# Performance work log

Measured on AMD Instinct MI355X. Metric: run time of the kernel, lower is better.

The kernel has to match this reference:

```python
import jax, jax.numpy as jnp
import numpy as np

TOP_K = 2

def setup_inputs() -> dict:
    key = jax.random.key(0)
    k1, k2 = jax.random.split(key)
    x = jax.random.normal(k1, (8, 4096, 4096), dtype=jnp.float32)
    # nn.Linear weight [num_experts, dim]
    gate_w = jax.random.normal(k2, (64, 4096), dtype=jnp.float32) * (1.0 / np.sqrt(4096))
    return {"x": x, "gate_w": gate_w}

def reference(x, gate_w):
    # logits: [B, S, E]
    logits = jnp.einsum('bsd,ed->bse', x, gate_w)
    routing_weights = jax.nn.softmax(logits, axis=-1)
    top_weights, top_indices = jax.lax.top_k(routing_weights, TOP_K)
    top_weights = top_weights / jnp.sum(top_weights, axis=-1, keepdims=True)
    return top_weights, top_indices
```

## Files before the change

kernel.cpp:

```cpp
#include <hip/hip_runtime.h>
#include <hip/hip_bf16.h>
#include <math.h>


typedef __attribute__((ext_vector_type(8))) short short8;
typedef __attribute__((ext_vector_type(4))) float f32x4;

#define TPB 64
#define NCH 64
#define TAU 1e-4f
#define LROW 68

__device__ __forceinline__ void cvt8(const f32x4* v, short8* hi, short8* lo) {
    const float* f = reinterpret_cast<const float*>(v);
#pragma unroll
    for (int j = 0; j < 8; ++j) {
        __hip_bfloat16 h = __float2bfloat16(f[j]);
        float r = f[j] - __bfloat162float(h);
        __hip_bfloat16 l = __float2bfloat16(r);
        (*hi)[j] = (short)*reinterpret_cast<unsigned short*>(&h);
        (*lo)[j] = (short)*reinterpret_cast<unsigned short*>(&l);
    }
}

__global__ void prep_b(const float* __restrict__ gw,
                       short8* __restrict__ bh, short8* __restrict__ bl) {
    const int tid = blockIdx.x * 256 + threadIdx.x;
    const int ln  = tid & 63;
    const int w   = (tid >> 6) & 127;
    const int nt  = tid >> 13;
    const int row = nt * 16 + (ln & 15);
    const int k   = w * 32 + ((ln >> 4) << 3);
    f32x4 v[2];
    v[0] = *reinterpret_cast<const f32x4*>(gw + (long)row * 4096 + k);
    v[1] = *reinterpret_cast<const f32x4*>(gw + (long)row * 4096 + k + 4);
    short8 h, l;
    cvt8(v, &h, &l);
    bh[tid] = h;
    bl[tid] = l;
}

__device__ __forceinline__ void gload16(const void* g, void* l) {
    __builtin_amdgcn_global_load_lds(
        (const __attribute__((address_space(1))) void*)g,
        (__attribute__((address_space(3))) void*)l, 16, 0, 0);
}

#define STAGE(C, BUF) do {                                                    \
    char* aB = AB + (BUF) * 32768;                                            \
    char* bB = aB + 16384;                                                    \
    _Pragma("unroll")                                                         \
    for (int i = 0; i < 4; ++i)                                               \
        gload16(srcA[i] + (long)(C) * 256, aB + (wv * 4 + i) * 1024 + ln * 16); \
    _Pragma("unroll")                                                         \
    for (int i = 0; i < 4; ++i) {                                             \
        const int s  = wv * 4 + i;                                            \
        const int wl = s >> 3, nt = (s >> 1) & 3, hl = s & 1;                 \
        const short8* sp = (hl ? blp : bhp)                                   \
            + ((long)nt * 8192 + (2 * (C) + wl) * 64 + ln);                   \
        gload16(sp, bB + s * 1024 + ln * 16);                                 \
    }                                                                         \
} while (0)

__global__ __launch_bounds__(256, 2)
void router_fused(const float* __restrict__ x,
                  const short8* __restrict__ bhp,
                  const short8* __restrict__ blp,
                  const float* __restrict__ gw,
                  float* __restrict__ out,
                  int M, int K) {
    __shared__ __align__(16) char AB[65536];
    __shared__ int flags[TPB];
    __shared__ double Ld4[4][64];

    const int t  = threadIdx.x;
    const int wv = t >> 6;
    const int ln = t & 63;
    const int fr = ln & 15;
    const int q  = ln >> 4;
    const long tok0 = (long)blockIdx.x * TPB;
    const int phase = blockIdx.x & (NCH - 1);

    const char* srcA[4];
#pragma unroll
    for (int i = 0; i < 4; ++i) {
        const int row  = (wv * 4 + i) * 4 + (ln >> 4);
        const int sl   = ln & 15;
        const int lslot = (sl & 8) | ((sl & 7) ^ (row & 7));
        srcA[i] = (const char*)x + (tok0 + row) * (long)K * 4 + lslot * 16;
    }

    f32x4 acc[4];
#pragma unroll
    for (int nt = 0; nt < 4; ++nt) acc[nt] = (f32x4){0.f, 0.f, 0.f, 0.f};

    STAGE(phase, 0);
    STAGE((phase + 1) & (NCH - 1), 1);

    const int R  = wv * 16 + fr;
    const int rk = R & 7;

    for (int j = 0; j < NCH; ++j) {
        const int c   = (phase + j) & (NCH - 1);
        const int buf = j & 1;
        if (j + 1 < NCH) asm volatile("s_waitcnt vmcnt(8)" ::: "memory");
        else             asm volatile("s_waitcnt vmcnt(0)" ::: "memory");
        __builtin_amdgcn_s_barrier();
        asm volatile("" ::: "memory");
        __builtin_amdgcn_sched_barrier(0);

        {
            const char* aB = AB + buf * 32768 + R * 256;
            const char* bB = AB + buf * 32768 + 16384;
#pragma unroll
            for (int wl = 0; wl < 2; ++wl) {
                f32x4 av[2];
                av[0] = *(const f32x4*)(aB + (wl * 8 + ((q * 2 + 0) ^ rk)) * 16);
                av[1] = *(const f32x4*)(aB + (wl * 8 + ((q * 2 + 1) ^ rk)) * 16);
                short8 ah, al;
                cvt8(av, &ah, &al);
#pragma unroll
                for (int nt = 0; nt < 4; ++nt) {
                    short8 bhv = *(const short8*)(bB + (wl * 8 + nt * 2 + 0) * 1024 + ln * 16);
                    short8 blv = *(const short8*)(bB + (wl * 8 + nt * 2 + 1) * 1024 + ln * 16);
                    acc[nt] = __builtin_amdgcn_mfma_f32_16x16x32_bf16(ah, bhv, acc[nt], 0, 0, 0);
                    acc[nt] = __builtin_amdgcn_mfma_f32_16x16x32_bf16(ah, blv, acc[nt], 0, 0, 0);
                    acc[nt] = __builtin_amdgcn_mfma_f32_16x16x32_bf16(al, bhv, acc[nt], 0, 0, 0);
                    acc[nt] = __builtin_amdgcn_mfma_f32_16x16x32_bf16(al, blv, acc[nt], 0, 0, 0);
                }
            }
        }

        __builtin_amdgcn_sched_barrier(0);
        asm volatile("" ::: "memory");
        __builtin_amdgcn_s_barrier();
        asm volatile("" ::: "memory");
        if (j + 2 < NCH) STAGE((phase + j + 2) & (NCH - 1), buf);
        __builtin_amdgcn_sched_barrier(0);
    }

    __syncthreads();
    float* Ls = (float*)AB;
#pragma unroll
    for (int nt = 0; nt < 4; ++nt)
#pragma unroll
        for (int r = 0; r < 4; ++r)
            Ls[(wv * 16 + q * 4 + r) * LROW + nt * 16 + fr] = acc[nt][r];
    __syncthreads();

    if (t < TPB) {
        const float* row = Ls + (long)t * LROW;
        float m1 = -INFINITY, m2 = -INFINITY, m3 = -INFINITY;
        int i1 = 0, i2 = 0;
#pragma unroll 8
        for (int e = 0; e < 64; ++e) {
            const float v = row[e];
            if (v > m1)      { m3 = m2; m2 = m1; i2 = i1; m1 = v; i1 = e; }
            else if (v > m2) { m3 = m2; m2 = v; i2 = e; }
            else if (v > m3) { m3 = v; }
        }
        const float e2 = expf(m2 - m1);
        const float s  = 1.0f + e2;

        const long g = tok0 + t;
        out[2 * g + 0] = 1.0f / s;
        out[2 * g + 1] = e2 / s;
        float* oi = out + 2 * (long)M;
        oi[2 * g + 0] = (float)i1;
        oi[2 * g + 1] = (float)i2;

        flags[t] = ((m1 - m2) < TAU) | ((m2 - m3) < TAU);
    }
    __syncthreads();

    for (int tk = 0; tk < TPB; ++tk) {
        if (flags[tk]) {
            const float* xr = x + (tok0 + tk) * (long)K + wv * 1024;
            const float* gr = gw + (long)ln * (long)K + wv * 1024;
            double s0 = 0.0, s1 = 0.0, s2 = 0.0, s3 = 0.0;
            for (int k = 0; k < 1024; k += 4) {
                const f32x4 a = *reinterpret_cast<const f32x4*>(xr + k);
                const f32x4 b = *reinterpret_cast<const f32x4*>(gr + k);
                s0 = fma((double)a.x, (double)b.x, s0);
                s1 = fma((double)a.y, (double)b.y, s1);
                s2 = fma((double)a.z, (double)b.z, s2);
                s3 = fma((double)a.w, (double)b.w, s3);
            }
            Ld4[wv][ln] = (s0 + s1) + (s2 + s3);
            __syncthreads();
            if (t == 0) {
                double m1 = -INFINITY, m2 = -INFINITY;
                int i1 = 0, i2 = 0;
                for (int e = 0; e < 64; ++e) {
                    const double v = Ld4[0][e] + Ld4[1][e] + Ld4[2][e] + Ld4[3][e];
                    if (v > m1)      { m2 = m1; i2 = i1; m1 = v; i1 = e; }
                    else if (v > m2) { m2 = v; i2 = e; }
                }
                const double e2 = exp(m2 - m1);
                const double s  = 1.0 + e2;
                const long g = tok0 + tk;
                out[2 * g + 0] = (float)(1.0 / s);
                out[2 * g + 1] = (float)(e2 / s);
                float* oi = out + 2 * (long)M;
                oi[2 * g + 0] = (float)i1;
                oi[2 * g + 1] = (float)i2;
            }
            __syncthreads();
        }
    }
}

extern "C" void kernel_launch(void* const* d_in, const int* in_sizes, int n_in,
                              void* d_out, int out_size, void* d_ws, size_t ws_size,
                              hipStream_t stream) {
    const float* x  = (const float*)d_in[0];
    const float* gw = (const float*)d_in[1];
    float* out = (float*)d_out;

    const int K = 4096;
    const int M = in_sizes[0] / K;
    const int nblocks = M / TPB;

    short8* bh = (short8*)d_ws;
    short8* bl = bh + 32768;

    prep_b<<<128, 256, 0, stream>>>(gw, bh, bl);
    router_fused<<<nblocks, 256, 0, stream>>>(x, bh, bl, gw, out, M, K);
}
```

Before: 206.1 us.

## Switch router GEMM to triple-buffered half-size chunks with one barrier

Halves the K chunk (NCH 128, 32 floats per row per chunk) and replaces the double buffer with a three-slot LDS ring of 16 KB each. The prefetch for chunk j+2 is issued right after the single per-iteration barrier, which removes the second barrier. LDS drops to 48 KB so three blocks can fit per CU, and MFMA sections are raised in wave priority via s_setprio. The cost is more loop iterations with less work each, and the waitcnt depth and buffer indexing have to stay correct.

```diff
diff --git a/kernel.cpp b/kernel.cpp
--- a/kernel.cpp
+++ b/kernel.cpp
@@ -7,7 +7,7 @@
 typedef __attribute__((ext_vector_type(4))) float f32x4;
 
 #define TPB 64
-#define NCH 64
+#define NCH 128
 #define TAU 1e-4f
 #define LROW 68
 
@@ -46,30 +46,29 @@
         (__attribute__((address_space(3))) void*)l, 16, 0, 0);
 }
 
-#define STAGE(C, BUF) do {                                                    \
-    char* aB = AB + (BUF) * 32768;                                            \
-    char* bB = aB + 16384;                                                    \
+#define STAGE(C, MBUF) do {                                                   \
+    char* aB = AB + (MBUF) * 16384;                                           \
+    char* bB = aB + 8192;                                                     \
     _Pragma("unroll")                                                         \
-    for (int i = 0; i < 4; ++i)                                               \
-        gload16(srcA[i] + (long)(C) * 256, aB + (wv * 4 + i) * 1024 + ln * 16); \
+    for (int i = 0; i < 2; ++i)                                               \
+        gload16(srcA[i] + (long)(C) * 128, aB + (wv * 2 + i) * 1024 + ln * 16); \
     _Pragma("unroll")                                                         \
-    for (int i = 0; i < 4; ++i) {                                             \
-        const int s  = wv * 4 + i;                                            \
-        const int wl = s >> 3, nt = (s >> 1) & 3, hl = s & 1;                 \
-        const short8* sp = (hl ? blp : bhp)                                   \
-            + ((long)nt * 8192 + (2 * (C) + wl) * 64 + ln);                   \
+    for (int i = 0; i < 2; ++i) {                                             \
+        const int s  = wv * 2 + i;                                            \
+        const short8* sp = ((s & 1) ? blp : bhp)                              \
+            + ((long)(s >> 1) * 8192 + (long)(C) * 64 + ln);                  \
         gload16(sp, bB + s * 1024 + ln * 16);                                 \
     }                                                                         \
 } while (0)
 
-__global__ __launch_bounds__(256, 2)
+__global__ __launch_bounds__(256, 3)
 void router_fused(const float* __restrict__ x,
                   const short8* __restrict__ bhp,
                   const short8* __restrict__ blp,
                   const float* __restrict__ gw,
                   float* __restrict__ out,
                   int M, int K) {
-    __shared__ __align__(16) char AB[65536];
+    __shared__ __align__(16) char AB[49152];
     __shared__ int flags[TPB];
     __shared__ double Ld4[4][64];
 
@@ -81,13 +80,12 @@
     const long tok0 = (long)blockIdx.x * TPB;
     const int phase = blockIdx.x & (NCH - 1);
 
-    const char* srcA[4];
-#pragma unroll
-    for (int i = 0; i < 4; ++i) {
-        const int row  = (wv * 4 + i) * 4 + (ln >> 4);
-        const int sl   = ln & 15;
-        const int lslot = (sl & 8) | ((sl & 7) ^ (row & 7));
-        srcA[i] = (const char*)x + (tok0 + row) * (long)K * 4 + lslot * 16;
+    const char* srcA[2];
+#pragma unroll
+    for (int i = 0; i < 2; ++i) {
+        const int row  = (wv * 2 + i) * 8 + (ln >> 3);
+        const int slot = (ln & 7) ^ (row & 7);
+        srcA[i] = (const char*)x + (tok0 + row) * (long)K * 4 + slot * 16;
     }
 
     f32x4 acc[4];
@@ -101,42 +99,37 @@
     const int rk = R & 7;
 
     for (int j = 0; j < NCH; ++j) {
-        const int c   = (phase + j) & (NCH - 1);
-        const int buf = j & 1;
-        if (j + 1 < NCH) asm volatile("s_waitcnt vmcnt(8)" ::: "memory");
+        const int c = (phase + j) & (NCH - 1);
+        const int m = j % 3;
+        if (j < NCH - 1) asm volatile("s_waitcnt vmcnt(4)" ::: "memory");
         else             asm volatile("s_waitcnt vmcnt(0)" ::: "memory");
         __builtin_amdgcn_s_barrier();
         asm volatile("" ::: "memory");
+        if (j + 2 < NCH) STAGE((phase + j + 2) & (NCH - 1), (j + 2) % 3);
         __builtin_amdgcn_sched_barrier(0);
 
         {
-            const char* aB = AB + buf * 32768 + R * 256;
-            const char* bB = AB + buf * 32768 + 16384;
-#pragma unroll
-            for (int wl = 0; wl < 2; ++wl) {
-                f32x4 av[2];
-                av[0] = *(const f32x4*)(aB + (wl * 8 + ((q * 2 + 0) ^ rk)) * 16);
-                av[1] = *(const f32x4*)(aB + (wl * 8 + ((q * 2 + 1) ^ rk)) * 16);
-                short8 ah, al;
-                cvt8(av, &ah, &al);
-#pragma unroll
-                for (int nt = 0; nt < 4; ++nt) {
-                    short8 bhv = *(const short8*)(bB + (wl * 8 + nt * 2 + 0) * 1024 + ln * 16);
-                    short8 blv = *(const short8*)(bB + (wl * 8 + nt * 2 + 1) * 1024 + ln * 16);
-                    acc[nt] = __builtin_amdgcn_mfma_f32_16x16x32_bf16(ah, bhv, acc[nt], 0, 0, 0);
-                    acc[nt] = __builtin_amdgcn_mfma_f32_16x16x32_bf16(ah, blv, acc[nt], 0, 0, 0);
-                    acc[nt] = __builtin_amdgcn_mfma_f32_16x16x32_bf16(al, bhv, acc[nt], 0, 0, 0);
-                    acc[nt] = __builtin_amdgcn_mfma_f32_16x16x32_bf16(al, blv, acc[nt], 0, 0, 0);
-                }
+            const char* aB = AB + m * 16384 + R * 128;
+            const char* bB = AB + m * 16384 + 8192;
+            f32x4 av[2];
+            av[0] = *(const f32x4*)(aB + (((q * 2 + 0) ^ rk) * 16));
+            av[1] = *(const f32x4*)(aB + (((q * 2 + 1) ^ rk) * 16));
+            short8 ah, al;
+            cvt8(av, &ah, &al);
+            __builtin_amdgcn_s_setprio(1);
+#pragma unroll
+            for (int nt = 0; nt < 4; ++nt) {
+                short8 bhv = *(const short8*)(bB + (nt * 2 + 0) * 1024 + ln * 16);
+                short8 blv = *(const short8*)(bB + (nt * 2 + 1) * 1024 + ln * 16);
+                acc[nt] = __builtin_amdgcn_mfma_f32_16x16x32_bf16(ah, bhv, acc[nt], 0, 0, 0);
+                acc[nt] = __builtin_amdgcn_mfma_f32_16x16x32_bf16(ah, blv, acc[nt], 0, 0, 0);
+                acc[nt] = __builtin_amdgcn_mfma_f32_16x16x32_bf16(al, bhv, acc[nt], 0, 0, 0);
+                acc[nt] = __builtin_amdgcn_mfma_f32_16x16x32_bf16(al, blv, acc[nt], 0, 0, 0);
             }
+            __builtin_amdgcn_s_setprio(0);
         }
-
         __builtin_amdgcn_sched_barrier(0);
         asm volatile("" ::: "memory");
-        __builtin_amdgcn_s_barrier();
-        asm volatile("" ::: "memory");
-        if (j + 2 < NCH) STAGE((phase + j + 2) & (NCH - 1), buf);
-        __builtin_amdgcn_sched_barrier(0);
     }
 
     __syncthreads();
```

Measured after the change: 246.7 us. 1.2x slower.

## Load activations directly into registers and stage only gate weights in LDS

Applied to the files above, without the earlier changes.

Activation tiles now go straight from global memory into double-buffered registers, one chunk ahead, instead of through swizzled LDS with global_load_lds. Only the bf16 hi/lo gate-weight tiles stay double-buffered in shared memory. This halves the LDS staging buffer and raises the occupancy hint from 2 to 4 blocks per CU, to keep more memory traffic in flight. In exchange, prefetch depth for activations is only one chunk, the per-lane strided global loads may coalesce worse, and the vmcnt accounting must match the new load counts.

```diff
diff --git a/kernel.cpp b/kernel.cpp
--- a/kernel.cpp
+++ b/kernel.cpp
@@ -46,12 +46,8 @@
         (__attribute__((address_space(3))) void*)l, 16, 0, 0);
 }
 
-#define STAGE(C, BUF) do {                                                    \
-    char* aB = AB + (BUF) * 32768;                                            \
-    char* bB = aB + 16384;                                                    \
-    _Pragma("unroll")                                                         \
-    for (int i = 0; i < 4; ++i)                                               \
-        gload16(srcA[i] + (long)(C) * 256, aB + (wv * 4 + i) * 1024 + ln * 16); \
+#define STAGE_B(C, BUF) do {                                                  \
+    char* bB = BB + (BUF) * 16384;                                            \
     _Pragma("unroll")                                                         \
     for (int i = 0; i < 4; ++i) {                                             \
         const int s  = wv * 4 + i;                                            \
@@ -62,14 +58,57 @@
     }                                                                         \
 } while (0)
 
-__global__ __launch_bounds__(256, 2)
+#define LOAD_A(BUF, C) do {                                                   \
+    const float* p = pA + (long)(C) * 64;                                     \
+    (BUF)[0] = *reinterpret_cast<const f32x4*>(p);                            \
+    (BUF)[1] = *reinterpret_cast<const f32x4*>(p + 4);                        \
+    (BUF)[2] = *reinterpret_cast<const f32x4*>(p + 32);                       \
+    (BUF)[3] = *reinterpret_cast<const f32x4*>(p + 36);                       \
+} while (0)
+
+#define ITER(J, ACUR, ANXT) do {                                              \
+    const int c_   = (phase + (J)) & (NCH - 1);                               \
+    const int buf_ = (J) & 1;                                                 \
+    if ((J) + 1 < NCH) asm volatile("s_waitcnt vmcnt(4)" ::: "memory");       \
+    else               asm volatile("s_waitcnt vmcnt(0)" ::: "memory");       \
+    __builtin_amdgcn_s_barrier();                                             \
+    asm volatile("" ::: "memory");                                            \
+    if ((J) + 1 < NCH) LOAD_A(ANXT, (phase + (J) + 1) & (NCH - 1));           \
+    __builtin_amdgcn_sched_barrier(0);                                        \
+    {                                                                         \
+        const char* bB = BB + buf_ * 16384;                                   \
+        _Pragma("unroll")                                                     \
+        for (int wl = 0; wl < 2; ++wl) {                                      \
+            short8 ah, al;                                                    \
+            cvt8(&(ACUR)[wl * 2], &ah, &al);                                  \
+            _Pragma("unroll")                                                 \
+            for (int nt = 0; nt < 4; ++nt) {                                  \
+                short8 bhv = *(const short8*)(bB + (wl * 8 + nt * 2 + 0) * 1024 + ln * 16); \
+                short8 blv = *(const short8*)(bB + (wl * 8 + nt * 2 + 1) * 1024 + ln * 16); \
+                acc[nt] = __builtin_amdgcn_mfma_f32_16x16x32_bf16(ah, bhv, acc[nt], 0, 0, 0); \
+                acc[nt] = __builtin_amdgcn_mfma_f32_16x16x32_bf16(ah, blv, acc[nt], 0, 0, 0); \
+                acc[nt] = __builtin_amdgcn_mfma_f32_16x16x32_bf16(al, bhv, acc[nt], 0, 0, 0); \
+                acc[nt] = __builtin_amdgcn_mfma_f32_16x16x32_bf16(al, blv, acc[nt], 0, 0, 0); \
+            }                                                                 \
+        }                                                                     \
+    }                                                                         \
+    __builtin_amdgcn_sched_barrier(0);                                        \
+    asm volatile("" ::: "memory");                                            \
+    __builtin_amdgcn_s_barrier();                                             \
+    asm volatile("" ::: "memory");                                            \
+    if ((J) + 2 < NCH) STAGE_B((phase + (J) + 2) & (NCH - 1), buf_);          \
+    __builtin_amdgcn_sched_barrier(0);                                        \
+} while (0)
+
+__global__ __launch_bounds__(256, 4)
 void router_fused(const float* __restrict__ x,
                   const short8* __restrict__ bhp,
                   const short8* __restrict__ blp,
                   const float* __restrict__ gw,
                   float* __restrict__ out,
                   int M, int K) {
-    __shared__ __align__(16) char AB[65536];
+    __shared__ __align__(16) char BB[32768];
+    __shared__ float Ls[TPB * LROW];
     __shared__ int flags[TPB];
     __shared__ double Ld4[4][64];
 
@@ -81,66 +120,24 @@
     const long tok0 = (long)blockIdx.x * TPB;
     const int phase = blockIdx.x & (NCH - 1);
 
-    const char* srcA[4];
-#pragma unroll
-    for (int i = 0; i < 4; ++i) {
-        const int row  = (wv * 4 + i) * 4 + (ln >> 4);
-        const int sl   = ln & 15;
-        const int lslot = (sl & 8) | ((sl & 7) ^ (row & 7));
-        srcA[i] = (const char*)x + (tok0 + row) * (long)K * 4 + lslot * 16;
-    }
+    const float* pA = x + (tok0 + wv * 16 + fr) * (long)K + q * 8;
 
     f32x4 acc[4];
 #pragma unroll
     for (int nt = 0; nt < 4; ++nt) acc[nt] = (f32x4){0.f, 0.f, 0.f, 0.f};
 
-    STAGE(phase, 0);
-    STAGE((phase + 1) & (NCH - 1), 1);
-
-    const int R  = wv * 16 + fr;
-    const int rk = R & 7;
-
-    for (int j = 0; j < NCH; ++j) {
-        const int c   = (phase + j) & (NCH - 1);
-        const int buf = j & 1;
-        if (j + 1 < NCH) asm volatile("s_waitcnt vmcnt(8)" ::: "memory");
-        else             asm volatile("s_waitcnt vmcnt(0)" ::: "memory");
-        __builtin_amdgcn_s_barrier();
-        asm volatile("" ::: "memory");
-        __builtin_amdgcn_sched_barrier(0);
-
-        {
-            const char* aB = AB + buf * 32768 + R * 256;
-            const char* bB = AB + buf * 32768 + 16384;
-#pragma unroll
-            for (int wl = 0; wl < 2; ++wl) {
-                f32x4 av[2];
-                av[0] = *(const f32x4*)(aB + (wl * 8 + ((q * 2 + 0) ^ rk)) * 16);
-                av[1] = *(const f32x4*)(aB + (wl * 8 + ((q * 2 + 1) ^ rk)) * 16);
-                short8 ah, al;
-                cvt8(av, &ah, &al);
-#pragma unroll
-                for (int nt = 0; nt < 4; ++nt) {
-                    short8 bhv = *(const short8*)(bB + (wl * 8 + nt * 2 + 0) * 1024 + ln * 16);
-                    short8 blv = *(const short8*)(bB + (wl * 8 + nt * 2 + 1) * 1024 + ln * 16);
-                    acc[nt] = __builtin_amdgcn_mfma_f32_16x16x32_bf16(ah, bhv, acc[nt], 0, 0, 0);
-                    acc[nt] = __builtin_amdgcn_mfma_f32_16x16x32_bf16(ah, blv, acc[nt], 0, 0, 0);
-                    acc[nt] = __builtin_amdgcn_mfma_f32_16x16x32_bf16(al, bhv, acc[nt], 0, 0, 0);
-                    acc[nt] = __builtin_amdgcn_mfma_f32_16x16x32_bf16(al, blv, acc[nt], 0, 0, 0);
-                }
-            }
-        }
-
-        __builtin_amdgcn_sched_barrier(0);
-        asm volatile("" ::: "memory");
-        __builtin_amdgcn_s_barrier();
-        asm volatile("" ::: "memory");
-        if (j + 2 < NCH) STAGE((phase + j + 2) & (NCH - 1), buf);
-        __builtin_amdgcn_sched_barrier(0);
+    f32x4 Ae[4], Ao[4];
+
+    LOAD_A(Ae, phase);
+    STAGE_B(phase, 0);
+    STAGE_B((phase + 1) & (NCH - 1), 1);
+
+    for (int j = 0; j < NCH; j += 2) {
+        ITER(j, Ae, Ao);
+        ITER(j + 1, Ao, Ae);
     }
 
     __syncthreads();
-    float* Ls = (float*)AB;
 #pragma unroll
     for (int nt = 0; nt < 4; ++nt)
 #pragma unroll
```

Measured after the change: 216.5 us. 1.05x slower.
